# Optimization experiments

Measured on AMD Instinct MI355X. Metric: run time of the kernel, lower is better.

Reference implementation:

```python
import jax, jax.numpy as jnp
import numpy as np

C = 256
NUM_HEADS = 8
FFN_HIDDEN = C * 2  # ffn_expand=2
EPS = 1e-5


def setup_inputs() -> dict:
    key = jax.random.key(0)
    ks = jax.random.split(key, 12)
    B, H, W = 16, 64, 64
    s = 0.02
    return {
        "optical": jax.random.normal(ks[0], (B, C, H, W), jnp.float32),
        "sar": jax.random.normal(ks[1], (B, C, H, W), jnp.float32),
        "g_opt": jnp.ones((C,), jnp.float32),
        "b_opt": jnp.zeros((C,), jnp.float32),
        "g_sar": jnp.ones((C,), jnp.float32),
        "b_sar": jnp.zeros((C,), jnp.float32),
        "Wq": jax.random.normal(ks[2], (C, C), jnp.float32) * s,
        "Wk": jax.random.normal(ks[3], (C, C), jnp.float32) * s,
        "Wv": jax.random.normal(ks[4], (C, C), jnp.float32) * s,
        "Wo": jax.random.normal(ks[5], (C, C), jnp.float32) * s,
        "g_ffn": jnp.ones((C,), jnp.float32),
        "b_ffn": jnp.zeros((C,), jnp.float32),
        "W1": jax.random.normal(ks[6], (2 * FFN_HIDDEN, C), jnp.float32) * s,
        "b1": jnp.zeros((2 * FFN_HIDDEN,), jnp.float32),
        "W2": jax.random.normal(ks[7], (C, FFN_HIDDEN), jnp.float32) * s,
        "b2": jnp.zeros((C,), jnp.float32),
    }


def _ln(x, g, b):
    # LayerNorm over channel axis of (B, C, H, W), biased variance, eps=1e-5
    mu = jnp.mean(x, axis=1, keepdims=True)
    var = jnp.mean(jnp.square(x - mu), axis=1, keepdims=True)
    xn = (x - mu) * jax.lax.rsqrt(var + EPS)
    return xn * g[None, :, None, None] + b[None, :, None, None]


def _proj(x, Wmat):
    # 1x1 conv == channel matmul
    return jnp.einsum('oc,bchw->bohw', Wmat, x)


def reference(optical, sar, g_opt, b_opt, g_sar, b_sar, Wq, Wk, Wv, Wo,
              g_ffn, b_ffn, W1, b1, W2, b2):
    B, Cc, H, W = optical.shape
    hc = Cc // NUM_HEADS
    L = H * W
    scale = hc ** -0.5

    opt_n = _ln(optical, g_opt, b_opt)
    sar_n = _ln(sar, g_sar, b_sar)

    # channel (transposed) attention: contraction over spatial L
    q = _proj(opt_n, Wq).reshape(B, NUM_HEADS, hc, L)
    k = _proj(sar_n, Wk).reshape(B, NUM_HEADS, hc, L)
    v = _proj(sar_n, Wv).reshape(B, NUM_HEADS, hc, L)
    A = jax.nn.softmax(jnp.einsum('bhcl,bhdl->bhcd', q, k) * scale, axis=-1)
    attn = jnp.einsum('bhcd,bhdl->bhcl', A, v).reshape(B, Cc, H, W)
    x = optical + _proj(attn, Wo)

    # SimpleGate FFN
    h = _ln(x, g_ffn, b_ffn)
    h = _proj(h, W1) + b1[None, :, None, None]
    h1, h2 = jnp.split(h, 2, axis=1)
    h = _proj(h1 * h2, W2) + b2[None, :, None, None]
    return x + h
```

## Files before the change

kernel.cpp:

```cpp
#include <hip/hip_runtime.h>
#include <hip/hip_bf16.h>

typedef __bf16 bf16;
typedef __attribute__((ext_vector_type(8))) __bf16 bf16x8;
typedef __attribute__((ext_vector_type(4))) __bf16 bf16x4;
typedef __attribute__((ext_vector_type(4))) float f32x4;
typedef __attribute__((ext_vector_type(16))) float f32x16;

#define LSP 4096
#define CCH 256

__device__ __forceinline__ void gl2lds16(const bf16* g, bf16* l) {
  __builtin_amdgcn_global_load_lds(
      (const __attribute__((address_space(1))) unsigned int*)g,
      (__attribute__((address_space(3))) unsigned int*)l, 16, 0, 0);
}

__device__ __forceinline__ f32x4 mfma16(bf16x8 a, bf16x8 b, f32x4 c) {
  return __builtin_amdgcn_mfma_f32_16x16x32_bf16(a, b, c, 0, 0, 0);
}
__device__ __forceinline__ f32x16 mfma32(bf16x8 a, bf16x8 b, f32x16 c) {
  return __builtin_amdgcn_mfma_f32_32x32x16_bf16(a, b, c, 0, 0, 0);
}

__global__ __launch_bounds__(256) void cvt_w_kernel(
    const float* __restrict__ wq, const float* __restrict__ wk,
    const float* __restrict__ wv, const float* __restrict__ wo,
    const float* __restrict__ w1, const float* __restrict__ w2,
    bf16* __restrict__ out) {
  int e = blockIdx.x * 256 + threadIdx.x;
  if (e < 65536)        { out[e] = (bf16)wq[e]; }
  else if (e < 131072)  { out[e] = (bf16)wk[e - 65536]; }
  else if (e < 196608)  {
    int e2 = e - 131072;
    int och = e2 >> 8, cin = e2 & 255;
    out[131072 + cin * 256 + och] = (bf16)wv[e2];
  }
  else if (e < 262144)  { out[e] = (bf16)wo[e - 196608]; }
  else if (e < 524288)  {
    int e2 = e - 262144;
    int m = e2 >> 8, k = e2 & 255;
    int mp = (m < 512) ? (2 * m) : (2 * (m - 512) + 1);
    out[262144 + mp * 256 + k] = (bf16)w1[e2];
  }
  else                  { out[e] = (bf16)w2[e - 524288]; }
}

template <int DUAL>
__global__ __launch_bounds__(256) void ln_tile_kernel(
    const float* __restrict__ x, const float* __restrict__ gam,
    const float* __restrict__ bet, bf16* __restrict__ out_cl,
    bf16* __restrict__ out_lc) {
  const int l0 = blockIdx.x * 64;
  const int b  = blockIdx.y;
  const int tid = threadIdx.x;
  __shared__ bf16 Tt[256 * 64];
  __shared__ float red[2][16][64];
  __shared__ float mu_s[64], rs_s[64];

  const float* px = x + (size_t)b * CCH * LSP + l0;
  const int colq = (tid & 15) * 4;
  f32x4 s = {0.f, 0.f, 0.f, 0.f}, q = {0.f, 0.f, 0.f, 0.f};
  #pragma unroll
  for (int it = 0; it < 16; ++it) {
    int c = it * 16 + (tid >> 4);
    f32x4 v = *(const f32x4*)&px[(size_t)c * LSP + colq];
    s += v;
    q += v * v;
    bf16x4 h;
    #pragma unroll
    for (int j = 0; j < 4; ++j) h[j] = (bf16)v[j];
    int colp = colq ^ (((c >> 3) & 7) << 3);
    *(bf16x4*)&Tt[c * 64 + colp] = h;
  }
  #pragma unroll
  for (int j = 0; j < 4; ++j) {
    red[0][tid >> 4][colq + j] = s[j];
    red[1][tid >> 4][colq + j] = q[j];
  }
  __syncthreads();
  if (tid < 64) {
    float S = 0.f, Q = 0.f;
    #pragma unroll
    for (int k = 0; k < 16; ++k) { S += red[0][k][tid]; Q += red[1][k][tid]; }
    float m = S * (1.f / 256.f);
    mu_s[tid] = m;
    rs_s[tid] = rsqrtf(Q * (1.f / 256.f) - m * m + 1e-5f);
  }
  __syncthreads();

  #pragma unroll
  for (int it = 0; it < 8; ++it) {
    int ch = it * 256 + tid;
    int c = ch >> 3, col8 = (ch & 7) * 8;
    int colp = col8 ^ (((c >> 3) & 7) << 3);
    bf16x8 h = *(const bf16x8*)&Tt[c * 64 + colp];
    f32x4 m0 = *(const f32x4*)&mu_s[col8];
    f32x4 m1 = *(const f32x4*)&mu_s[col8 + 4];
    f32x4 r0 = *(const f32x4*)&rs_s[col8];
    f32x4 r1 = *(const f32x4*)&rs_s[col8 + 4];
    float g = gam[c], be = bet[c];
    bf16x8 o;
    #pragma unroll
    for (int j = 0; j < 4; ++j) {
      o[j]     = (bf16)(((float)h[j] - m0[j]) * r0[j] * g + be);
      o[4 + j] = (bf16)(((float)h[4 + j] - m1[j]) * r1[j] * g + be);
    }
    *(bf16x8*)&out_cl[((size_t)b * CCH + c) * LSP + l0 + col8] = o;
  }

  if constexpr (DUAL) {
    #pragma unroll
    for (int it = 0; it < 8; ++it) {
      int ch = it * 256 + tid;
      int l = ch >> 5, cch = ch & 31;
      int c0 = cch * 8;
      int lp = l ^ ((cch & 7) << 3);
      float mu = mu_s[l], rs = rs_s[l];
      f32x4 g0 = *(const f32x4*)&gam[c0];
      f32x4 g1 = *(const f32x4*)&gam[c0 + 4];
      f32x4 b0 = *(const f32x4*)&bet[c0];
      f32x4 b1 = *(const f32x4*)&bet[c0 + 4];
      bf16x8 o;
      #pragma unroll
      for (int j = 0; j < 4; ++j) {
        float h0 = (float)Tt[(c0 + j) * 64 + lp];
        float h1 = (float)Tt[(c0 + 4 + j) * 64 + lp];
        o[j]     = (bf16)((h0 - mu) * rs * g0[j] + b0[j]);
        o[4 + j] = (bf16)((h1 - mu) * rs * g1[j] + b1[j]);
      }
      *(bf16x8*)&out_lc[((size_t)b * LSP + l0 + l) * CCH + c0] = o;
    }
  }
}

__global__ __launch_bounds__(256) void gram_kernel(
    const bf16* __restrict__ sar_cl, const bf16* __restrict__ opt_cl,
    float* __restrict__ part) {
  const int tile = blockIdx.x, chunk = blockIdx.y, b = blockIdx.z;
  const int tid = threadIdx.x, lane = tid & 63, w = tid >> 6;
  const int j0 = (tile >> 1) * 128 + (w >> 1) * 64;
  const int i0 = (tile & 1) * 128 + (w & 1) * 64;
  const int l0 = chunk * 1024;
  const bf16* sj = sar_cl + ((size_t)b * CCH + j0 + (lane & 31)) * LSP + l0;
  const bf16* oi = opt_cl + ((size_t)b * CCH + i0 + (lane & 31)) * LSP + l0;
  f32x16 acc[2][2];
  #pragma unroll
  for (int mt = 0; mt < 2; ++mt)
    #pragma unroll
    for (int nt = 0; nt < 2; ++nt)
      #pragma unroll
      for (int r = 0; r < 16; ++r) acc[mt][nt][r] = 0.f;
  #pragma unroll 4
  for (int ks = 0; ks < 64; ++ks) {
    int lofs = ks * 16 + (lane >> 5) * 8;
    bf16x8 a0 = *(const bf16x8*)&sj[lofs];
    bf16x8 a1 = *(const bf16x8*)&sj[32 * LSP + lofs];
    bf16x8 b0 = *(const bf16x8*)&oi[lofs];
    bf16x8 b1 = *(const bf16x8*)&oi[32 * LSP + lofs];
    acc[0][0] = mfma32(a0, b0, acc[0][0]);
    acc[0][1] = mfma32(a0, b1, acc[0][1]);
    acc[1][0] = mfma32(a1, b0, acc[1][0]);
    acc[1][1] = mfma32(a1, b1, acc[1][1]);
  }
  float* op = part + ((size_t)chunk * 16 + b) * 65536;
  #pragma unroll
  for (int mt = 0; mt < 2; ++mt)
    #pragma unroll
    for (int nt = 0; nt < 2; ++nt)
      #pragma unroll
      for (int r = 0; r < 16; ++r) {
        int row = j0 + mt * 32 + (r & 3) + 8 * (r >> 2) + 4 * (lane >> 5);
        int col = i0 + nt * 32 + (lane & 31);
        op[(size_t)row * 256 + col] = acc[mt][nt][r];
      }
}

__global__ __launch_bounds__(256) void greduce_kernel(
    const float* __restrict__ part, bf16* __restrict__ G2) {
  size_t e = ((size_t)blockIdx.x * 256 + threadIdx.x) * 8;
  float a[8];
  #pragma unroll
  for (int i = 0; i < 8; ++i) a[i] = 0.f;
  #pragma unroll
  for (int ch = 0; ch < 4; ++ch) {
    f32x4 p0 = *(const f32x4*)&part[ch * 1048576ull + e];
    f32x4 p1 = *(const f32x4*)&part[ch * 1048576ull + e + 4];
    #pragma unroll
    for (int i = 0; i < 4; ++i) { a[i] += p0[i]; a[4 + i] += p1[i]; }
  }
  bf16x8 o;
  #pragma unroll
  for (int i = 0; i < 8; ++i) o[i] = (bf16)a[i];
  *(bf16x8*)&G2[e] = o;
}

__global__ __launch_bounds__(256) void fold2_kernel(
    const bf16* __restrict__ G2, const bf16* __restrict__ Wq,
    const bf16* __restrict__ Wk, const bf16* __restrict__ WvT,
    bf16* __restrict__ UT) {
  const int bh = blockIdx.x;
  const int b = bh >> 3, h = bh & 7;
  const int tid = threadIdx.x, lane = tid & 63, w = tid >> 6;
  __shared__ bf16 M1[32 * 256];
  __shared__ float Sp[4][1024];
  __shared__ float S[1024];
  __shared__ bf16 P[1024];

  const bf16* gq = Wq + (size_t)(h * 32) * 256;
  const bf16* g2b = G2 + (size_t)b * 65536;
  #pragma unroll
  for (int mt = 0; mt < 2; ++mt)
    #pragma unroll
    for (int nt = 0; nt < 4; ++nt) {
      f32x4 acc = {0.f, 0.f, 0.f, 0.f};
      #pragma unroll
      for (int ks = 0; ks < 8; ++ks) {
        bf16x8 a = *(const bf16x8*)&gq[(size_t)(mt * 16 + (lane & 15)) * 256 +
                                       ks * 32 + (lane >> 4) * 8];
        bf16x8 bb = *(const bf16x8*)&g2b[
            (size_t)(w * 64 + nt * 16 + (lane & 15)) * 256 + ks * 32 +
            (lane >> 4) * 8];
        acc = mfma16(a, bb, acc);
      }
      #pragma unroll
      for (int r = 0; r < 4; ++r)
        M1[(mt * 16 + (lane >> 4) * 4 + r) * 256 + w * 64 + nt * 16 +
           (lane & 15)] = (bf16)acc[r];
    }
  __syncthreads();

  const bf16* gk = Wk + (size_t)(h * 32) * 256;
  #pragma unroll
  for (int mt = 0; mt < 2; ++mt)
    #pragma unroll
    for (int dt = 0; dt < 2; ++dt) {
      f32x4 acc = {0.f, 0.f, 0.f, 0.f};
      #pragma unroll
      for (int kk = 0; kk < 2; ++kk) {
        bf16x8 a = *(const bf16x8*)&M1[(mt * 16 + (lane & 15)) * 256 + w * 64 +
                                       kk * 32 + (lane >> 4) * 8];
        bf16x8 bb = *(const bf16x8*)&gk[(size_t)(dt * 16 + (lane & 15)) * 256 +
                                        w * 64 + kk * 32 + (lane >> 4) * 8];
        acc = mfma16(a, bb, acc);
      }
      #pragma unroll
      for (int r = 0; r < 4; ++r)
        Sp[w][(mt * 16 + (lane >> 4) * 4 + r) * 32 + dt * 16 + (lane & 15)] =
            acc[r];
    }
  __syncthreads();
  #pragma unroll
  for (int i = 0; i < 4; ++i) {
    int e = tid + 256 * i;
    S[e] = (Sp[0][e] + Sp[1][e] + Sp[2][e] + Sp[3][e]) * 0.17677669529663687f;
  }
  __syncthreads();
  if (tid < 32) {
    float m = -1e30f;
    #pragma unroll
    for (int d = 0; d < 32; ++d) m = fmaxf(m, S[tid * 32 + d]);
    float sum = 0.f;
    float ex[32];
    #pragma unroll
    for (int d = 0; d < 32; ++d) {
      ex[d] = __expf(S[tid * 32 + d] - m);
      sum += ex[d];
    }
    float inv = 1.f / sum;
    #pragma unroll
    for (int d = 0; d < 32; ++d) P[tid * 32 + d] = (bf16)(ex[d] * inv);
  }
  __syncthreads();

  bf16x8 bfrag[2];
  #pragma unroll
  for (int ct = 0; ct < 2; ++ct)
    bfrag[ct] =
        *(const bf16x8*)&P[(ct * 16 + (lane & 15)) * 32 + (lane >> 4) * 8];
  bf16* outb = UT + (size_t)b * 65536 + h * 32;
  #pragma unroll
  for (int t = 0; t < 4; ++t) {
    int cin16 = w * 64 + t * 16;
    bf16x8 afrag = *(const bf16x8*)&WvT[(size_t)(cin16 + (lane & 15)) * 256 +
                                        h * 32 + (lane >> 4) * 8];
    #pragma unroll
    for (int ct = 0; ct < 2; ++ct) {
      f32x4 acc = {0.f, 0.f, 0.f, 0.f};
      acc = mfma16(afrag, bfrag[ct], acc);
      int c = ct * 16 + (lane & 15);
      int cinr = cin16 + (lane >> 4) * 4;
      #pragma unroll
      for (int r = 0; r < 4; ++r)
        outb[(size_t)(cinr + r) * 256 + c] = (bf16)acc[r];
    }
  }
}

__global__ __launch_bounds__(256) void wfold_kernel(
    const bf16* __restrict__ Aw, const bf16* __restrict__ Bx,
    bf16* __restrict__ outp) {
  const int tid = threadIdx.x;
  const int lane = tid & 63;
  const int wave = tid >> 6;
  const int wr = wave >> 1, wc = wave & 1;
  const int l0 = blockIdx.x * 128;
  const int m0 = blockIdx.y * 128;
  const int b  = blockIdx.z;
  constexpr int NB = 4096;
  __shared__ bf16 smem[4 * NB];
  bf16* As = smem;
  bf16* Bs = smem + 2 * NB;
  const bf16* Ag = Aw + (size_t)m0 * 256;
  const bf16* Bg = Bx + ((size_t)b * 256 + l0) * 256;
  auto stage = [&](int buf, int k0) {
    #pragma unroll
    for (int i = 0; i < 2; ++i) {
      int ch = i * 256 + tid;
      int r  = ch >> 2;
      int c8 = (ch & 3) * 8;
      gl2lds16(Ag + (size_t)r * 256 + k0 + c8, As + buf * NB + ch * 8);
      gl2lds16(Bg + (size_t)r * 256 + k0 + c8, Bs + buf * NB + ch * 8);
    }
  };
  f32x4 acc[4][4];
  #pragma unroll
  for (int mi = 0; mi < 4; ++mi)
    #pragma unroll
    for (int ni = 0; ni < 4; ++ni)
      #pragma unroll
      for (int r = 0; r < 4; ++r) acc[mi][ni][r] = 0.f;
  stage(0, 0);
  for (int kt = 0; kt < 8; ++kt) {
    __syncthreads();
    if (kt + 1 < 8) stage((kt + 1) & 1, (kt + 1) * 32);
    const bf16* Ab = As + (kt & 1) * NB;
    const bf16* Bb = Bs + (kt & 1) * NB;
    bf16x8 af[4], bfr[4];
    #pragma unroll
    for (int mi = 0; mi < 4; ++mi)
      af[mi] = *(const bf16x8*)&Ab[(wr * 64 + mi * 16 + (lane & 15)) * 32 +
                                   (lane >> 4) * 8];
    #pragma unroll
    for (int ni = 0; ni < 4; ++ni)
      bfr[ni] = *(const bf16x8*)&Bb[(wc * 64 + ni * 16 + (lane & 15)) * 32 +
                                    (lane >> 4) * 8];
    #pragma unroll
    for (int mi = 0; mi < 4; ++mi)
      #pragma unroll
      for (int ni = 0; ni < 4; ++ni)
        acc[mi][ni] = mfma16(af[mi], bfr[ni], acc[mi][ni]);
  }
  const int mq = m0 + wr * 64 + (lane >> 4) * 4;
  const int lq = l0 + wc * 64 + (lane & 15);
  #pragma unroll
  for (int mi = 0; mi < 4; ++mi)
    #pragma unroll
    for (int ni = 0; ni < 4; ++ni) {
      int l = lq + ni * 16, mb = mq + mi * 16;
      #pragma unroll
      for (int r = 0; r < 4; ++r)
        outp[((size_t)b * 256 + mb + r) * 256 + l] = (bf16)acc[mi][ni][r];
    }
}

__global__ __launch_bounds__(256) void xgemm_ln_kernel(
    const bf16* __restrict__ Wfold, const bf16* __restrict__ sar_lc,
    const float* __restrict__ optical, const float* __restrict__ gff,
    const float* __restrict__ bff, float* __restrict__ xbuf,
    bf16* __restrict__ hn) {
  const int tid = threadIdx.x, lane = tid & 63, w = tid >> 6;
  const int l0 = blockIdx.x * 64;
  const int b  = blockIdx.y;
  __shared__ bf16 As[2][256 * 32];
  __shared__ bf16 Bs[2][64 * 32];
  __shared__ float red[2][4][64];

  const bf16* Ag = Wfold + (size_t)b * 65536;
  const bf16* Bg = sar_lc + ((size_t)b * LSP + l0) * CCH;

  auto stage = [&](int buf, int k0) {
    #pragma unroll
    for (int i = 0; i < 4; ++i) {
      int ch = i * 256 + tid;
      int r = ch >> 2, c8 = (ch & 3) * 8;
      gl2lds16(Ag + (size_t)r * 256 + k0 + c8, &As[buf][ch * 8]);
    }
    {
      int r = tid >> 2, c8 = (tid & 3) * 8;
      gl2lds16(Bg + (size_t)r * 256 + k0 + c8, &Bs[buf][tid * 8]);
    }
  };

  f32x4 acc[4][4];
  #pragma unroll
  for (int mi = 0; mi < 4; ++mi)
    #pragma unroll
    for (int ni = 0; ni < 4; ++ni)
      #pragma unroll
      for (int r = 0; r < 4; ++r) acc[mi][ni][r] = 0.f;

  stage(0, 0);
  for (int kt = 0; kt < 8; ++kt) {
    __syncthreads();
    if (kt < 7) stage((kt + 1) & 1, (kt + 1) * 32);
    const bf16* Ab = As[kt & 1];
    const bf16* Bb = Bs[kt & 1];
    bf16x8 af[4], bfr[4];
    #pragma unroll
    for (int mi = 0; mi < 4; ++mi)
      af[mi] = *(const bf16x8*)&Ab[(w * 64 + mi * 16 + (lane & 15)) * 32 +
                                   (lane >> 4) * 8];
    #pragma unroll
    for (int ni = 0; ni < 4; ++ni)
      bfr[ni] = *(const bf16x8*)&Bs[kt & 1][(ni * 16 + (lane & 15)) * 32 +
                                            (lane >> 4) * 8];
    #pragma unroll
    for (int mi = 0; mi < 4; ++mi)
      #pragma unroll
      for (int ni = 0; ni < 4; ++ni)
        acc[mi][ni] = mfma16(af[mi], bfr[ni], acc[mi][ni]);
    (void)Bb;
  }

  const int cb = w * 64 + (lane >> 4) * 4;
  const int lb = l0 + (lane & 15);
  float s[4], q[4];
  #pragma unroll
  for (int ni = 0; ni < 4; ++ni) { s[ni] = 0.f; q[ni] = 0.f; }
  #pragma unroll
  for (int mi = 0; mi < 4; ++mi)
    #pragma unroll
    for (int ni = 0; ni < 4; ++ni) {
      int c = cb + mi * 16, l = lb + ni * 16;
      #pragma unroll
      for (int r = 0; r < 4; ++r) {
        float v = acc[mi][ni][r] + optical[((size_t)b * CCH + c + r) * LSP + l];
        acc[mi][ni][r] = v;
        s[ni] += v; q[ni] += v * v;
      }
    }
  #pragma unroll
  for (int ni = 0; ni < 4; ++ni) {
    s[ni] += __shfl_xor(s[ni], 16);
    s[ni] += __shfl_xor(s[ni], 32);
    q[ni] += __shfl_xor(q[ni], 16);
    q[ni] += __shfl_xor(q[ni], 32);
  }
  if ((lane >> 4) == 0) {
    #pragma unroll
    for (int ni = 0; ni < 4; ++ni) {
      red[0][w][ni * 16 + (lane & 15)] = s[ni];
      red[1][w][ni * 16 + (lane & 15)] = q[ni];
    }
  }
  __syncthreads();
  float mu[4], rsg[4];
  #pragma unroll
  for (int ni = 0; ni < 4; ++ni) {
    int ll = ni * 16 + (lane & 15);
    float S4 = red[0][0][ll] + red[0][1][ll] + red[0][2][ll] + red[0][3][ll];
    float Q4 = red[1][0][ll] + red[1][1][ll] + red[1][2][ll] + red[1][3][ll];
    float m = S4 * (1.f / 256.f);
    mu[ni] = m;
    rsg[ni] = rsqrtf(Q4 * (1.f / 256.f) - m * m + 1e-5f);
  }
  #pragma unroll
  for (int mi = 0; mi < 4; ++mi) {
    int c = cb + mi * 16;
    f32x4 g4 = *(const f32x4*)&gff[c];
    f32x4 b4 = *(const f32x4*)&bff[c];
    #pragma unroll
    for (int ni = 0; ni < 4; ++ni) {
      int l = lb + ni * 16;
      f32x4 xv = acc[mi][ni];
      *(f32x4*)&xbuf[((size_t)b * LSP + l) * CCH + c] = xv;
      bf16x4 o;
      #pragma unroll
      for (int r = 0; r < 4; ++r)
        o[r] = (bf16)((xv[r] - mu[ni]) * rsg[ni] * g4[r] + b4[r]);
      *(bf16x4*)&hn[((size_t)b * LSP + l) * CCH + c] = o;
    }
  }
}

template <int KEL, int MODE>
__global__ __launch_bounds__(512, 2) void ffn_gemm_kernel(
    const bf16* __restrict__ Aw, const bf16* __restrict__ Bx,
    void* __restrict__ outp, const float* __restrict__ res,
    const float* __restrict__ bias) {
  constexpr int LDSB = (MODE == 1) ? 135168 : 131072;
  __shared__ __align__(16) char smem_raw[LDSB];
  const int tid = threadIdx.x;
  const int lane = tid & 63;
  const int wave = tid >> 6;
  const int wr = wave >> 2;
  const int wc = wave & 3;
  const int l0 = blockIdx.x * 256;
  const int m0 = blockIdx.y * 256;
  const int b  = blockIdx.z;

  char* ldsA0 = smem_raw;
  char* ldsB0 = smem_raw + 32768;
  char* ldsA1 = smem_raw + 65536;
  char* ldsB1 = smem_raw + 98304;

  const bf16* Ag = Aw + (size_t)m0 * KEL;
  const bf16* Bg = Bx + ((size_t)b * LSP + l0) * KEL;

  auto STAGE = [&](const bf16* gsrc, char* ldst, int par, int kt) {
    #pragma unroll
    for (int i = 0; i < 2; ++i) {
      int qi = i * 512 + tid;
      int r  = ((qi >> 7) << 5) + (par << 4) + ((qi >> 3) & 15);
      int cl = (qi & 7) ^ ((qi >> 3) & 7);
      int p  = ((qi >> 7) << 8) + (par << 7) + (qi & 127);
      gl2lds16(gsrc + (size_t)r * KEL + kt * 64 + cl * 8,
               (bf16*)(ldst + p * 16));
    }
  };

  f32x4 acc[8][4];
  #pragma unroll
  for (int mi = 0; mi < 8; ++mi)
    #pragma unroll
    for (int ni = 0; ni < 4; ++ni)
      #pragma unroll
      for (int r = 0; r < 4; ++r) acc[mi][ni][r] = 0.f;

  bf16x8 af[4][2], bf[2][2];
  const int col0 = (((lane >> 4) << 4)) ^ ((lane & 7) << 4);
  const int col1 = col0 ^ 64;
  const int arow_off = (lane & 15) * 128;

#define LOAD_FRAGS(BUFA, BUFB, MP, NP)                                        \
  {                                                                           \
    const char* Ab_ = (BUFA);                                                 \
    const char* Bb_ = (BUFB);                                                 \
    _Pragma("unroll") for (int j = 0; j < 4; ++j) {                           \
      int rb = (wr * 128 + ((MP) + 2 * j) * 16) * 128 + arow_off;             \
      af[j][0] = *(const bf16x8*)(Ab_ + rb + col0);                           \
      af[j][1] = *(const bf16x8*)(Ab_ + rb + col1);                           \
    }                                                                         \
    _Pragma("unroll") for (int i = 0; i < 2; ++i) {                           \
      int rb = (wc * 64 + ((NP) + 2 * i) * 16) * 128 + arow_off;              \
      bf[i][0] = *(const bf16x8*)(Bb_ + rb + col0);                           \
      bf[i][1] = *(const bf16x8*)(Bb_ + rb + col1);                           \
    }                                                                         \
  }

#define DO_MFMA(MP, NP)                                                       \
  _Pragma("unroll") for (int j = 0; j < 4; ++j)                               \
  _Pragma("unroll") for (int i = 0; i < 2; ++i) {                             \
    acc[(MP) + 2 * j][(NP) + 2 * i] =                                         \
        mfma16(af[j][0], bf[i][0], acc[(MP) + 2 * j][(NP) + 2 * i]);          \
    acc[(MP) + 2 * j][(NP) + 2 * i] =                                         \
        mfma16(af[j][1], bf[i][1], acc[(MP) + 2 * j][(NP) + 2 * i]);          \
  }

#define PHASE(BUFA, BUFB, MP, NP, STG)                                        \
  asm volatile("s_waitcnt vmcnt(6)" ::: "memory");                            \
  __builtin_amdgcn_s_barrier();                                               \
  __builtin_amdgcn_sched_barrier(0);                                          \
  LOAD_FRAGS(BUFA, BUFB, MP, NP);                                             \
  STG;                                                                        \
  asm volatile("s_waitcnt lgkmcnt(0)" ::: "memory");                          \
  __builtin_amdgcn_sched_barrier(0);                                          \
  __builtin_amdgcn_s_setprio(1);                                              \
  DO_MFMA(MP, NP);                                                            \
  __builtin_amdgcn_s_setprio(0);

  STAGE(Ag, ldsA0, 0, 0);
  STAGE(Ag, ldsA0, 1, 0);
  STAGE(Bg, ldsB0, 0, 0);
  STAGE(Bg, ldsB0, 1, 0);
  STAGE(Ag, ldsA1, 0, 1);
  STAGE(Bg, ldsB1, 0, 1);

  constexpr int NITER = KEL / 128;
  for (int t = 0; t < NITER; ++t) {
    const int kt1 = 2 * t + 1;
    PHASE(ldsA0, ldsB0, 0, 0, STAGE(Ag, ldsA1, 1, kt1));
    PHASE(ldsA0, ldsB0, 0, 1, STAGE(Bg, ldsB1, 1, kt1));
    PHASE(ldsA0, ldsB0, 1, 0, STAGE(Ag, ldsA0, 0, kt1 + 1));
    PHASE(ldsA0, ldsB0, 1, 1, STAGE(Bg, ldsB0, 0, kt1 + 1));
    PHASE(ldsA1, ldsB1, 0, 0, STAGE(Ag, ldsA0, 1, kt1 + 1));
    PHASE(ldsA1, ldsB1, 0, 1, STAGE(Bg, ldsB0, 1, kt1 + 1));
    PHASE(ldsA1, ldsB1, 1, 0, STAGE(Ag, ldsA1, 0, kt1 + 2));
    PHASE(ldsA1, ldsB1, 1, 1, STAGE(Bg, ldsB1, 0, kt1 + 2));
  }
#undef PHASE
#undef DO_MFMA
#undef LOAD_FRAGS

  asm volatile("s_waitcnt vmcnt(0)" ::: "memory");
  __syncthreads();

  if constexpr (MODE == 0) {
    bf16* g_lds = (bf16*)smem_raw;
    const int lq = wc * 64 + (lane & 15);
    const int qq = (lane >> 4);
    #pragma unroll
    for (int mi = 0; mi < 8; ++mi) {
      int a0 = wr * 64 + mi * 8 + qq * 2;
      int ag = (m0 >> 1) + a0;
      float b10 = bias[ag], b1h0 = bias[ag + 512];
      float b11 = bias[ag + 1], b1h1 = bias[ag + 1 + 512];
      #pragma unroll
      for (int ni = 0; ni < 4; ++ni) {
        int l = lq + ni * 16;
        float g0 = (acc[mi][ni][0] + b10) * (acc[mi][ni][1] + b1h0);
        float g1 = (acc[mi][ni][2] + b11) * (acc[mi][ni][3] + b1h1);
        bf16 gv0 = (bf16)g0, gv1 = (bf16)g1;
        unsigned u = ((unsigned)*(unsigned short*)&gv1 << 16) |
                     (unsigned)*(unsigned short*)&gv0;
        *(unsigned*)&g_lds[l * 136 + a0] = u;
      }
    }
    __syncthreads();
    bf16* out = (bf16*)outp;
    const int gy = blockIdx.y * 128;
    #pragma unroll
    for (int it = 0; it < 8; ++it) {
      int cid = it * 512 + tid;
      int l = cid >> 4, ch = cid & 15;
      bf16x8 v = *(const bf16x8*)&g_lds[l * 136 + ch * 8];
      *(bf16x8*)&out[((size_t)b * LSP + l0 + l) * 512 + gy + ch * 8] = v;
    }
  } else {
    float* lds_f = (float*)smem_raw;
    float* out = (float*)outp;
    const int lq = wc * 64 + (lane & 15);
    const int qq = (lane >> 4);
    #pragma unroll
    for (int round = 0; round < 2; ++round) {
      if (wr == round) {
        #pragma unroll
        for (int mi = 0; mi < 8; ++mi) {
          int c0 = mi * 16 + qq * 4;
          f32x4 b4 = *(const f32x4*)&bias[round * 128 + c0];
          #pragma unroll
          for (int ni = 0; ni < 4; ++ni) {
            int l = lq + ni * 16;
            f32x4 xr = *(const f32x4*)&res[((size_t)b * LSP + l0 + l) * CCH +
                                           round * 128 + c0];
            #pragma unroll
            for (int r = 0; r < 4; ++r)
              lds_f[(c0 + r) * 260 + l] = acc[mi][ni][r] + b4[r] + xr[r];
          }
        }
      }
      __syncthreads();
      #pragma unroll
      for (int it = 0; it < 16; ++it) {
        int cid = it * 512 + tid;
        int c = cid >> 6, lch = cid & 63;
        f32x4 v = *(const f32x4*)&lds_f[c * 260 + lch * 4];
        *(f32x4*)&out[((size_t)b * CCH + round * 128 + c) * LSP + l0 +
                      lch * 4] = v;
      }
      __syncthreads();
    }
  }
}

extern "C" void kernel_launch(void* const* d_in, const int* in_sizes, int n_in,
                              void* d_out, int out_size, void* d_ws,
                              size_t ws_size, hipStream_t stream) {
  const float* optical = (const float*)d_in[0];
  const float* sar     = (const float*)d_in[1];
  const float* g_opt   = (const float*)d_in[2];
  const float* b_opt   = (const float*)d_in[3];
  const float* g_sar   = (const float*)d_in[4];
  const float* b_sar   = (const float*)d_in[5];
  const float* Wq      = (const float*)d_in[6];
  const float* Wk      = (const float*)d_in[7];
  const float* Wv      = (const float*)d_in[8];
  const float* Wo      = (const float*)d_in[9];
  const float* g_ffn   = (const float*)d_in[10];
  const float* b_ffn   = (const float*)d_in[11];
  const float* W1      = (const float*)d_in[12];
  const float* b1      = (const float*)d_in[13];
  const float* W2      = (const float*)d_in[14];
  const float* b2      = (const float*)d_in[15];

  char* ws = (char*)d_ws;
  bf16* wbf  = (bf16*)ws;
  bf16* Wqb  = wbf;
  bf16* Wkb  = wbf + 65536;
  bf16* WvTb = wbf + 131072;
  bf16* Wob  = wbf + 196608;
  bf16* W1b  = wbf + 262144;
  bf16* W2b  = wbf + 524288;

  size_t off = 2ull * 1024 * 1024;
  const size_t T16 = 16ull * LSP * CCH * 2;
  bf16* opt_ncl = (bf16*)(ws + off); off += T16;
  bf16* sar_ncl = (bf16*)(ws + off); off += T16;
  bf16* sar_nlc = (bf16*)(ws + off); off += T16;
  bf16* hn      = (bf16*)(ws + off); off += T16;
  float* xbuf   = (float*)(ws + off); off += 2 * T16;
  float* Gpart  = (float*)(ws + off); off += 16ull * 1024 * 1024;
  bf16* G2b     = (bf16*)(ws + off); off += 4ull * 1024 * 1024;
  bf16* UTb     = (bf16*)(ws + off); off += 2ull * 1024 * 1024;
  bf16* Wfoldb  = (bf16*)(ws + off); off += 2ull * 1024 * 1024;
  bf16* gbuf = opt_ncl;

  dim3 blk(256);
  cvt_w_kernel<<<2560, blk, 0, stream>>>(Wq, Wk, Wv, Wo, W1, W2, wbf);
  ln_tile_kernel<0><<<dim3(64, 16), blk, 0, stream>>>(optical, g_opt, b_opt,
                                                      opt_ncl, nullptr);
  ln_tile_kernel<1><<<dim3(64, 16), blk, 0, stream>>>(sar, g_sar, b_sar,
                                                      sar_ncl, sar_nlc);
  gram_kernel<<<dim3(4, 4, 16), blk, 0, stream>>>(sar_ncl, opt_ncl, Gpart);
  greduce_kernel<<<512, blk, 0, stream>>>(Gpart, G2b);
  fold2_kernel<<<128, blk, 0, stream>>>(G2b, Wqb, Wkb, WvTb, UTb);
  wfold_kernel<<<dim3(2, 2, 16), blk, 0, stream>>>(Wob, UTb, Wfoldb);
  xgemm_ln_kernel<<<dim3(64, 16), blk, 0, stream>>>(Wfoldb, sar_nlc, optical,
                                                    g_ffn, b_ffn, xbuf, hn);
  ffn_gemm_kernel<256, 0><<<dim3(16, 4, 16), dim3(512), 0, stream>>>(
      W1b, hn, gbuf, nullptr, b1);
  ffn_gemm_kernel<512, 1><<<dim3(16, 1, 16), dim3(512), 0, stream>>>(
      W2b, gbuf, (float*)d_out, xbuf, b2);
}
```

Before: 281.7 us.

## Fold FFN LayerNorm into W1 GEMM epilogue and store x as bf16

The FFN LayerNorm is folded algebraically: gamma is multiplied into W1, and per-row W1·beta and W1·gamma vectors are precomputed. The x-GEMM kernel now emits only the raw bf16 x plus per-pixel mean and rstd, and the W1 GEMM epilogue applies the normalisation. This removes the separate normalized hn tensor and the fp32 xbuf, cutting write and read traffic. In exchange, the residual x is kept in bf16, which lowers accuracy, and W1 now acts on unnormalised x rounded to bf16, which adds mean-subtraction cancellation error.

Measured after the change: 259.6 us. 1.09x faster.

```diff
diff --git a/kernel.cpp b/kernel.cpp
--- a/kernel.cpp
+++ b/kernel.cpp
@@ -27,7 +27,7 @@
     const float* __restrict__ wq, const float* __restrict__ wk,
     const float* __restrict__ wv, const float* __restrict__ wo,
     const float* __restrict__ w1, const float* __restrict__ w2,
-    bf16* __restrict__ out) {
+    const float* __restrict__ gff, bf16* __restrict__ out) {
   int e = blockIdx.x * 256 + threadIdx.x;
   if (e < 65536)        { out[e] = (bf16)wq[e]; }
   else if (e < 131072)  { out[e] = (bf16)wk[e - 65536]; }
@@ -41,9 +41,33 @@
     int e2 = e - 262144;
     int m = e2 >> 8, k = e2 & 255;
     int mp = (m < 512) ? (2 * m) : (2 * (m - 512) + 1);
-    out[262144 + mp * 256 + k] = (bf16)w1[e2];
+    out[262144 + mp * 256 + k] = (bf16)(w1[e2] * gff[k]);
   }
   else                  { out[e] = (bf16)w2[e - 524288]; }
+}
+
+__global__ __launch_bounds__(256) void w1vec_kernel(
+    const float* __restrict__ w1, const float* __restrict__ b1,
+    const float* __restrict__ gff, const float* __restrict__ bff,
+    float* __restrict__ cvec) {
+  int m = blockIdx.x * 256 + threadIdx.x;
+  const float* row = w1 + (size_t)m * 256;
+  float sb = 0.f, sg = 0.f;
+  #pragma unroll 8
+  for (int c = 0; c < 256; c += 4) {
+    f32x4 w = *(const f32x4*)&row[c];
+    f32x4 g = *(const f32x4*)&gff[c];
+    f32x4 bb = *(const f32x4*)&bff[c];
+    #pragma unroll
+    for (int j = 0; j < 4; ++j) { sb += w[j] * bb[j]; sg += w[j] * g[j]; }
+  }
+  if (m < 512) {
+    cvec[m] = sb + b1[m];
+    cvec[512 + m] = sg;
+  } else {
+    cvec[512 + m] = sb + b1[m];
+    cvec[1024 + m] = sg;
+  }
 }
 
 template <int DUAL>
@@ -364,31 +388,32 @@
     }
 }
 
-__global__ __launch_bounds__(256) void xgemm_ln_kernel(
+__global__ __launch_bounds__(256) void xgemm_stats_kernel(
     const bf16* __restrict__ Wfold, const bf16* __restrict__ sar_lc,
-    const float* __restrict__ optical, const float* __restrict__ gff,
-    const float* __restrict__ bff, float* __restrict__ xbuf,
-    bf16* __restrict__ hn) {
+    const float* __restrict__ optical, bf16* __restrict__ xout,
+    float* __restrict__ stats) {
   const int tid = threadIdx.x, lane = tid & 63, w = tid >> 6;
   const int l0 = blockIdx.x * 64;
   const int b  = blockIdx.y;
-  __shared__ bf16 As[2][256 * 32];
-  __shared__ bf16 Bs[2][64 * 32];
-  __shared__ float red[2][4][64];
+  __shared__ __align__(16) char smem[43520];
+  bf16* X = (bf16*)smem;
+  float* red = (float*)(smem + 40960);
 
   const bf16* Ag = Wfold + (size_t)b * 65536;
   const bf16* Bg = sar_lc + ((size_t)b * LSP + l0) * CCH;
 
   auto stage = [&](int buf, int k0) {
+    bf16* As = (bf16*)(smem + buf * 16384);
+    bf16* Bs = (bf16*)(smem + 32768 + buf * 4096);
     #pragma unroll
     for (int i = 0; i < 4; ++i) {
       int ch = i * 256 + tid;
       int r = ch >> 2, c8 = (ch & 3) * 8;
-      gl2lds16(Ag + (size_t)r * 256 + k0 + c8, &As[buf][ch * 8]);
+      gl2lds16(Ag + (size_t)r * 256 + k0 + c8, &As[ch * 8]);
     }
     {
       int r = tid >> 2, c8 = (tid & 3) * 8;
-      gl2lds16(Bg + (size_t)r * 256 + k0 + c8, &Bs[buf][tid * 8]);
+      gl2lds16(Bg + (size_t)r * 256 + k0 + c8, &Bs[tid * 8]);
     }
   };
 
@@ -404,8 +429,8 @@
   for (int kt = 0; kt < 8; ++kt) {
     __syncthreads();
     if (kt < 7) stage((kt + 1) & 1, (kt + 1) * 32);
-    const bf16* Ab = As[kt & 1];
-    const bf16* Bb = Bs[kt & 1];
+    const bf16* Ab = (const bf16*)(smem + (kt & 1) * 16384);
+    const bf16* Bb = (const bf16*)(smem + 32768 + (kt & 1) * 4096);
     bf16x8 af[4], bfr[4];
     #pragma unroll
     for (int mi = 0; mi < 4; ++mi)
@@ -413,18 +438,18 @@
                                    (lane >> 4) * 8];
     #pragma unroll
     for (int ni = 0; ni < 4; ++ni)
-      bfr[ni] = *(const bf16x8*)&Bs[kt & 1][(ni * 16 + (lane & 15)) * 32 +
-                                            (lane >> 4) * 8];
+      bfr[ni] = *(const bf16x8*)&Bb[(ni * 16 + (lane & 15)) * 32 +
+                                    (lane >> 4) * 8];
     #pragma unroll
     for (int mi = 0; mi < 4; ++mi)
       #pragma unroll
       for (int ni = 0; ni < 4; ++ni)
         acc[mi][ni] = mfma16(af[mi], bfr[ni], acc[mi][ni]);
-    (void)Bb;
-  }
+  }
+  __syncthreads();
 
   const int cb = w * 64 + (lane >> 4) * 4;
-  const int lb = l0 + (lane & 15);
+  const int lb = lane & 15;
   float s[4], q[4];
   #pragma unroll
   for (int ni = 0; ni < 4; ++ni) { s[ni] = 0.f; q[ni] = 0.f; }
@@ -432,13 +457,16 @@
   for (int mi = 0; mi < 4; ++mi)
     #pragma unroll
     for (int ni = 0; ni < 4; ++ni) {
-      int c = cb + mi * 16, l = lb + ni * 16;
+      int c = cb + mi * 16, ll = lb + ni * 16;
+      bf16x4 hx;
       #pragma unroll
       for (int r = 0; r < 4; ++r) {
-        float v = acc[mi][ni][r] + optical[((size_t)b * CCH + c + r) * LSP + l];
-        acc[mi][ni][r] = v;
+        float v = acc[mi][ni][r] +
+                  optical[((size_t)b * CCH + c + r) * LSP + l0 + ll];
         s[ni] += v; q[ni] += v * v;
+        hx[r] = (bf16)v;
       }
+      *(bf16x4*)&X[ll * 260 + c] = hx;
     }
   #pragma unroll
   for (int ni = 0; ni < 4; ++ni) {
@@ -450,45 +478,37 @@
   if ((lane >> 4) == 0) {
     #pragma unroll
     for (int ni = 0; ni < 4; ++ni) {
-      red[0][w][ni * 16 + (lane & 15)] = s[ni];
-      red[1][w][ni * 16 + (lane & 15)] = q[ni];
-    }
-  }
-  __syncthreads();
-  float mu[4], rsg[4];
-  #pragma unroll
-  for (int ni = 0; ni < 4; ++ni) {
-    int ll = ni * 16 + (lane & 15);
-    float S4 = red[0][0][ll] + red[0][1][ll] + red[0][2][ll] + red[0][3][ll];
-    float Q4 = red[1][0][ll] + red[1][1][ll] + red[1][2][ll] + red[1][3][ll];
+      red[(0 * 4 + w) * 64 + ni * 16 + lb] = s[ni];
+      red[(4 + w) * 64 + ni * 16 + lb] = q[ni];
+    }
+  }
+  __syncthreads();
+  if (tid < 64) {
+    float S4 = red[0 * 64 + tid] + red[1 * 64 + tid] + red[2 * 64 + tid] +
+               red[3 * 64 + tid];
+    float Q4 = red[4 * 64 + tid] + red[5 * 64 + tid] + red[6 * 64 + tid] +
+               red[7 * 64 + tid];
     float m = S4 * (1.f / 256.f);
-    mu[ni] = m;
-    rsg[ni] = rsqrtf(Q4 * (1.f / 256.f) - m * m + 1e-5f);
-  }
-  #pragma unroll
-  for (int mi = 0; mi < 4; ++mi) {
-    int c = cb + mi * 16;
-    f32x4 g4 = *(const f32x4*)&gff[c];
-    f32x4 b4 = *(const f32x4*)&bff[c];
-    #pragma unroll
-    for (int ni = 0; ni < 4; ++ni) {
-      int l = lb + ni * 16;
-      f32x4 xv = acc[mi][ni];
-      *(f32x4*)&xbuf[((size_t)b * LSP + l) * CCH + c] = xv;
-      bf16x4 o;
-      #pragma unroll
-      for (int r = 0; r < 4; ++r)
-        o[r] = (bf16)((xv[r] - mu[ni]) * rsg[ni] * g4[r] + b4[r]);
-      *(bf16x4*)&hn[((size_t)b * LSP + l) * CCH + c] = o;
-    }
+    float rs = rsqrtf(Q4 * (1.f / 256.f) - m * m + 1e-5f);
+    float* st = stats + ((size_t)b * LSP + l0 + tid) * 2;
+    st[0] = m;
+    st[1] = rs;
+  }
+  __syncthreads();
+  #pragma unroll
+  for (int it = 0; it < 8; ++it) {
+    int cid = it * 256 + tid;
+    int l = cid >> 5, c0 = (cid & 31) * 8;
+    bf16x8 v = *(const bf16x8*)&X[l * 260 + c0];
+    *(bf16x8*)&xout[((size_t)b * LSP + l0 + l) * CCH + c0] = v;
   }
 }
 
 template <int KEL, int MODE>
 __global__ __launch_bounds__(512, 2) void ffn_gemm_kernel(
     const bf16* __restrict__ Aw, const bf16* __restrict__ Bx,
-    void* __restrict__ outp, const float* __restrict__ res,
-    const float* __restrict__ bias) {
+    void* __restrict__ outp, const bf16* __restrict__ resb,
+    const float* __restrict__ bias, const float* __restrict__ stats) {
   constexpr int LDSB = (MODE == 1) ? 135168 : 131072;
   __shared__ __align__(16) char smem_raw[LDSB];
   const int tid = threadIdx.x;
@@ -600,18 +620,31 @@
     bf16* g_lds = (bf16*)smem_raw;
     const int lq = wc * 64 + (lane & 15);
     const int qq = (lane >> 4);
+    const float* stb = stats + ((size_t)b * LSP + l0) * 2;
+    float muv[4], rsv[4];
+    #pragma unroll
+    for (int ni = 0; ni < 4; ++ni) {
+      int l = lq + ni * 16;
+      muv[ni] = stb[l * 2];
+      rsv[ni] = stb[l * 2 + 1];
+    }
     #pragma unroll
     for (int mi = 0; mi < 8; ++mi) {
       int a0 = wr * 64 + mi * 8 + qq * 2;
       int ag = (m0 >> 1) + a0;
-      float b10 = bias[ag], b1h0 = bias[ag + 512];
-      float b11 = bias[ag + 1], b1h1 = bias[ag + 1 + 512];
+      float be1a = bias[ag],        ga1a = bias[512 + ag];
+      float be2a = bias[1024 + ag], ga2a = bias[1536 + ag];
+      float be1b = bias[ag + 1],        ga1b = bias[512 + ag + 1];
+      float be2b = bias[1024 + ag + 1], ga2b = bias[1536 + ag + 1];
       #pragma unroll
       for (int ni = 0; ni < 4; ++ni) {
         int l = lq + ni * 16;
-        float g0 = (acc[mi][ni][0] + b10) * (acc[mi][ni][1] + b1h0);
-        float g1 = (acc[mi][ni][2] + b11) * (acc[mi][ni][3] + b1h1);
-        bf16 gv0 = (bf16)g0, gv1 = (bf16)g1;
+        float mrs = muv[ni] * rsv[ni];
+        float h1a = rsv[ni] * acc[mi][ni][0] + be1a - mrs * ga1a;
+        float h2a = rsv[ni] * acc[mi][ni][1] + be2a - mrs * ga2a;
+        float h1b = rsv[ni] * acc[mi][ni][2] + be1b - mrs * ga1b;
+        float h2b = rsv[ni] * acc[mi][ni][3] + be2b - mrs * ga2b;
+        bf16 gv0 = (bf16)(h1a * h2a), gv1 = (bf16)(h1b * h2b);
         unsigned u = ((unsigned)*(unsigned short*)&gv1 << 16) |
                      (unsigned)*(unsigned short*)&gv0;
         *(unsigned*)&g_lds[l * 136 + a0] = u;
@@ -642,11 +675,12 @@
           #pragma unroll
           for (int ni = 0; ni < 4; ++ni) {
             int l = lq + ni * 16;
-            f32x4 xr = *(const f32x4*)&res[((size_t)b * LSP + l0 + l) * CCH +
-                                           round * 128 + c0];
+            bf16x4 xr4 = *(const bf16x4*)&resb[((size_t)b * LSP + l0 + l) *
+                                                   CCH + round * 128 + c0];
             #pragma unroll
             for (int r = 0; r < 4; ++r)
-              lds_f[(c0 + r) * 260 + l] = acc[mi][ni][r] + b4[r] + xr[r];
+              lds_f[(c0 + r) * 260 + l] =
+                  acc[mi][ni][r] + b4[r] + (float)xr4[r];
           }
         }
       }
@@ -698,8 +732,9 @@
   bf16* opt_ncl = (bf16*)(ws + off); off += T16;
   bf16* sar_ncl = (bf16*)(ws + off); off += T16;
   bf16* sar_nlc = (bf16*)(ws + off); off += T16;
-  bf16* hn      = (bf16*)(ws + off); off += T16;
-  float* xbuf   = (float*)(ws + off); off += 2 * T16;
+  bf16* xb      = (bf16*)(ws + off); off += T16;
+  float* stats  = (float*)(ws + off); off += 1ull * 1024 * 1024;
+  float* cvec   = (float*)(ws + off); off += 64 * 1024;
   float* Gpart  = (float*)(ws + off); off += 16ull * 1024 * 1024;
   bf16* G2b     = (bf16*)(ws + off); off += 4ull * 1024 * 1024;
   bf16* UTb     = (bf16*)(ws + off); off += 2ull * 1024 * 1024;
@@ -707,7 +742,8 @@
   bf16* gbuf = opt_ncl;
 
   dim3 blk(256);
-  cvt_w_kernel<<<2560, blk, 0, stream>>>(Wq, Wk, Wv, Wo, W1, W2, wbf);
+  cvt_w_kernel<<<2560, blk, 0, stream>>>(Wq, Wk, Wv, Wo, W1, W2, g_ffn, wbf);
+  w1vec_kernel<<<4, blk, 0, stream>>>(W1, b1, g_ffn, b_ffn, cvec);
   ln_tile_kernel<0><<<dim3(64, 16), blk, 0, stream>>>(optical, g_opt, b_opt,
                                                       opt_ncl, nullptr);
   ln_tile_kernel<1><<<dim3(64, 16), blk, 0, stream>>>(sar, g_sar, b_sar,
@@ -716,10 +752,10 @@
   greduce_kernel<<<512, blk, 0, stream>>>(Gpart, G2b);
   fold2_kernel<<<128, blk, 0, stream>>>(G2b, Wqb, Wkb, WvTb, UTb);
   wfold_kernel<<<dim3(2, 2, 16), blk, 0, stream>>>(Wob, UTb, Wfoldb);
-  xgemm_ln_kernel<<<dim3(64, 16), blk, 0, stream>>>(Wfoldb, sar_nlc, optical,
-                                                    g_ffn, b_ffn, xbuf, hn);
+  xgemm_stats_kernel<<<dim3(64, 16), blk, 0, stream>>>(Wfoldb, sar_nlc,
+                                                       optical, xb, stats);
   ffn_gemm_kernel<256, 0><<<dim3(16, 4, 16), dim3(512), 0, stream>>>(
-      W1b, hn, gbuf, nullptr, b1);
+      W1b, xb, gbuf, nullptr, cvec, stats);
   ffn_gemm_kernel<512, 1><<<dim3(16, 1, 16), dim3(512), 0, stream>>>(
-      W2b, gbuf, (float*)d_out, xbuf, b2);
-}
+      W2b, gbuf, (float*)d_out, xb, b2, nullptr);
+}
```
